# Kernel optimization log

Hardware: AMD Instinct MI355X
Metric: run time of the kernel (lower is better)

The kernel has to match this reference:

```python
import jax, jax.numpy as jnp
import numpy as np

CH = 64
INTER = 8  # max(64 // 8, 1)


def setup_inputs() -> dict:
    key = jax.random.key(0)
    ks = jax.random.split(key, 8)
    B, C, H, W = 4, CH, 64, 64
    x = jax.random.normal(ks[0], (B, C, H, W), dtype=jnp.float32)
    s = 1.0 / np.sqrt(C)
    Wq = jax.random.normal(ks[1], (INTER, C), dtype=jnp.float32) * s
    bq = jnp.zeros((INTER,), dtype=jnp.float32)
    Wk = jax.random.normal(ks[2], (INTER, C), dtype=jnp.float32) * s
    bk = jnp.zeros((INTER,), dtype=jnp.float32)
    Wv = jax.random.normal(ks[3], (C, C), dtype=jnp.float32) * s
    bv = jnp.zeros((C,), dtype=jnp.float32)
    gamma = jax.random.normal(ks[4], (1,), dtype=jnp.float32) * 0.1
    return {"x": x, "Wq": Wq, "bq": bq, "Wk": Wk, "bk": bk, "Wv": Wv, "bv": bv, "gamma": gamma}


def reference(x, Wq, bq, Wk, bk, Wv, bv, gamma):
    B, C, H, W = x.shape
    xf = x.reshape(B, C, H * W)  # [B, C, N]
    # 1x1 convs == per-pixel linear projections
    q = jnp.einsum('dc,bcn->bdn', Wq, xf) + bq[None, :, None]  # [B, d, N]
    k = jnp.einsum('dc,bcn->bdn', Wk, xf) + bk[None, :, None]  # [B, d, N]
    v = jnp.einsum('ec,bcn->ben', Wv, xf) + bv[None, :, None]  # [B, C, N]
    scale = 1.0 / np.sqrt(INTER).astype(np.float32)
    scores = jnp.einsum('bdi,bdj->bij', q, k) * scale  # [B, N, N]
    attn = jax.nn.softmax(scores, axis=-1)
    out = jnp.einsum('bcj,bij->bci', v, attn)  # value @ attn^T
    out = out.reshape(B, C, H, W)
    return gamma[0] * out + x
```

## Files before the change

### kernel.cpp

```cpp
#include <hip/hip_runtime.h>
#include <hip/hip_bf16.h>
#include <stdint.h>

#define BATCH 4
#define CCH   64
#define NPIX  4096
#define DQK   8

typedef __attribute__((ext_vector_type(8)))  short bf16x8;
typedef __attribute__((ext_vector_type(16))) float f32x16;

static __device__ __forceinline__ short f2bf(float f) {
    union { __hip_bfloat16 h; short s; } u;
    u.h = __float2bfloat16(f);
    return u.s;
}

__global__ __launch_bounds__(256) void proj_kernel(
    const float* __restrict__ x,
    const float* __restrict__ Wq, const float* __restrict__ bq,
    const float* __restrict__ Wk, const float* __restrict__ bk,
    const float* __restrict__ Wv, const float* __restrict__ bv,
    short* __restrict__ qo, short* __restrict__ ko, short* __restrict__ vo)
{
    __shared__ float xs[CCH][64];
    __shared__ float wv_s[CCH][CCH];
    __shared__ float wq_s[CCH][DQK];
    __shared__ float wk_s[CCH][DQK];

    const int b  = blockIdx.x >> 6;
    const int n0 = (blockIdx.x & 63) << 6;
    const int tid = threadIdx.x;

    for (int i = tid; i < CCH*CCH; i += 256) wv_s[i & 63][i >> 6] = Wv[i];
    for (int i = tid; i < CCH*DQK; i += 256) { wq_s[i & 63][i >> 6] = Wq[i]; wk_s[i & 63][i >> 6] = Wk[i]; }
    for (int i = tid; i < CCH*64; i += 256) {
        int c = i >> 6, p = i & 63;
        xs[c][p] = x[((size_t)b*CCH + c)*NPIX + n0 + p];
    }
    __syncthreads();

    const int p = tid & 63;
    const int g = tid >> 6;
    const int e0 = g * 16, d0 = g * 2;

    float av[16];
    #pragma unroll
    for (int i = 0; i < 16; ++i) av[i] = bv[e0 + i];
    float aq0 = bq[d0], aq1 = bq[d0+1];
    float ak0 = bk[d0], ak1 = bk[d0+1];

    for (int c = 0; c < CCH; ++c) {
        float xv = xs[c][p];
        const float4* wrow = (const float4*)&wv_s[c][e0];
        #pragma unroll
        for (int q4 = 0; q4 < 4; ++q4) {
            float4 w = wrow[q4];
            av[q4*4+0] += w.x * xv;
            av[q4*4+1] += w.y * xv;
            av[q4*4+2] += w.z * xv;
            av[q4*4+3] += w.w * xv;
        }
        float2 q2 = *(const float2*)&wq_s[c][d0];
        float2 k2 = *(const float2*)&wk_s[c][d0];
        aq0 += q2.x * xv; aq1 += q2.y * xv;
        ak0 += k2.x * xv; ak1 += k2.y * xv;
    }

    const float scale = 0.35355339059327373f;
    const size_t vb = (size_t)b * CCH * NPIX;
    #pragma unroll
    for (int i = 0; i < 16; ++i)
        vo[vb + (size_t)(e0 + i)*NPIX + n0 + p] = f2bf(av[i]);
    const size_t qb = ((size_t)b*NPIX + n0 + p)*DQK + d0;
    qo[qb]   = f2bf(aq0 * scale);
    qo[qb+1] = f2bf(aq1 * scale);
    ko[qb]   = f2bf(ak0);
    ko[qb+1] = f2bf(ak1);
}

__global__ __launch_bounds__(256) void attn_kernel(
    const short* __restrict__ qg, const short* __restrict__ kg,
    const short* __restrict__ vg,
    const float* __restrict__ x, const float* __restrict__ gamma,
    float* __restrict__ outp)
{
    __shared__ float m_s[4][32];
    __shared__ float l_s[4][32];
    __shared__ float acc_s[64][32];
    __shared__ __align__(16) short ps_s[4][32*40];

    const int b  = blockIdx.x >> 7;
    const int i0 = (blockIdx.x & 127) << 5;
    const int tid  = threadIdx.x;
    const int wave = tid >> 6, lane = tid & 63;
    const int hi = lane >> 5, li = lane & 31;

    for (int i = tid; i < 64*32; i += 256) acc_s[i >> 5][i & 31] = 0.f;
    __syncthreads();

    bf16x8 zf;
    #pragma unroll
    for (int i = 0; i < 8; ++i) zf[i] = 0;
    f32x16 z16;
    #pragma unroll
    for (int r = 0; r < 16; ++r) z16[r] = 0.f;

    bf16x8 qf = zf;
    if (hi == 0) qf = *(const bf16x8*)&qg[((size_t)b*NPIX + i0 + li)*DQK];

    f32x16 acc0 = z16, acc1 = z16;
    float m_run = -1e30f, l_run = 0.f;
    short* psb = &ps_s[wave][0];
    const size_t kbase = (size_t)b * NPIX * DQK;
    const size_t vbase = (size_t)b * CCH * NPIX;

    const int jbeg = wave << 10, jend = jbeg + 1024;
    for (int j0 = jbeg; j0 < jend; j0 += 32) {
        bf16x8 ak = zf;
        if (hi == 0) ak = *(const bf16x8*)&kg[kbase + (size_t)(j0 + li)*DQK];
        f32x16 S = __builtin_amdgcn_mfma_f32_32x32x16_bf16(ak, qf, z16, 0, 0, 0);

        float mx = S[0];
        #pragma unroll
        for (int r = 1; r < 16; ++r) mx = fmaxf(mx, S[r]);
        mx = fmaxf(mx, __shfl_xor(mx, 32));
        float m_new = fmaxf(m_run, mx);
        float fr = __expf(m_run - m_new);
        float p[16], ts = 0.f;
        #pragma unroll
        for (int r = 0; r < 16; ++r) { p[r] = __expf(S[r] - m_new); ts += p[r]; }
        ts += __shfl_xor(ts, 32);
        l_run = l_run * fr + ts;
        m_run = m_new;
        #pragma unroll
        for (int r = 0; r < 16; ++r) { acc0[r] *= fr; acc1[r] *= fr; }

        #pragma unroll
        for (int rp = 0; rp < 8; ++rp) {
            int r = rp * 2;
            int j = (r & 3) + ((r >> 2) << 3) + (hi << 2);
            uint32_t pk = (uint32_t)(uint16_t)f2bf(p[r]) |
                          ((uint32_t)(uint16_t)f2bf(p[r+1]) << 16);
            *(uint32_t*)((char*)psb + li*80 + j*2) = pk;
        }

        #pragma unroll
        for (int sub = 0; sub < 2; ++sub) {
            bf16x8 bp = *(const bf16x8*)((char*)psb + li*80 + (sub*16 + hi*8)*2);
            const short* vrow = &vg[vbase + (size_t)li*NPIX + j0 + sub*16 + hi*8];
            bf16x8 av0 = *(const bf16x8*)vrow;
            bf16x8 av1 = *(const bf16x8*)(vrow + (size_t)32*NPIX);
            acc0 = __builtin_amdgcn_mfma_f32_32x32x16_bf16(av0, bp, acc0, 0, 0, 0);
            acc1 = __builtin_amdgcn_mfma_f32_32x32x16_bf16(av1, bp, acc1, 0, 0, 0);
        }
    }

    if (hi == 0) { m_s[wave][li] = m_run; l_s[wave][li] = l_run; }
    __syncthreads();
    float M = fmaxf(fmaxf(m_s[0][li], m_s[1][li]), fmaxf(m_s[2][li], m_s[3][li]));
    float F = __expf(m_run - M);
    for (int w = 0; w < 4; ++w) {
        if (wave == w) {
            #pragma unroll
            for (int r = 0; r < 16; ++r) {
                int crow = (r & 3) + ((r >> 2) << 3) + (hi << 2);
                acc_s[crow][li]      += acc0[r] * F;
                acc_s[crow + 32][li] += acc1[r] * F;
            }
        }
        __syncthreads();
    }

    const float g0 = gamma[0];
    for (int idx = tid; idx < 64*32; idx += 256) {
        int c = idx >> 5, i = idx & 31;
        float Mq = fmaxf(fmaxf(m_s[0][i], m_s[1][i]), fmaxf(m_s[2][i], m_s[3][i]));
        float L = l_s[0][i]*__expf(m_s[0][i]-Mq) + l_s[1][i]*__expf(m_s[1][i]-Mq)
                + l_s[2][i]*__expf(m_s[2][i]-Mq) + l_s[3][i]*__expf(m_s[3][i]-Mq);
        size_t gidx = vbase + (size_t)c*NPIX + i0 + i;
        outp[gidx] = g0 * (acc_s[c][i] / L) + x[gidx];
    }
}

extern "C" void kernel_launch(void* const* d_in, const int* in_sizes, int n_in,
                              void* d_out, int out_size, void* d_ws, size_t ws_size,
                              hipStream_t stream) {
    const float* x     = (const float*)d_in[0];
    const float* Wq    = (const float*)d_in[1];
    const float* bq    = (const float*)d_in[2];
    const float* Wk    = (const float*)d_in[3];
    const float* bk    = (const float*)d_in[4];
    const float* Wv    = (const float*)d_in[5];
    const float* bv    = (const float*)d_in[6];
    const float* gamma = (const float*)d_in[7];

    short* qo = (short*)d_ws;
    short* ko = qo + (size_t)BATCH*NPIX*DQK;
    short* vo = ko + (size_t)BATCH*NPIX*DQK;

    proj_kernel<<<BATCH*(NPIX/64), 256, 0, stream>>>(x, Wq, bq, Wk, bk, Wv, bv, qo, ko, vo);
    attn_kernel<<<BATCH*(NPIX/32), 256, 0, stream>>>(qo, ko, vo, x, gamma, (float*)d_out);
}
```

Baseline: 126.3 us.

## Rewrite attention with lazy rescaling, exp2 folding, MFMA row sums and register P

Rewrites the attention kernel. The softmax scale times log2(e) is folded into q so exp2 can be used, and the running max is only updated when a score exceeds a threshold; the max offset is folded into the QK MFMA through an extra k column. P is packed to bf16 in registers and swapped across half-waves with permlane32_swap, which removes the LDS round trip. Row sums come from an extra MFMA against a ones vector. The block grows to 8 waves with a parallel cross-wave reduction in LDS, and the projection kernel is retiled to 32 pixels per block. The lazy-rescale threshold relies on scores staying bounded, which adds some numerical risk.

Measured after the change: 241.0 us. +90.8%, slower.

```diff
diff --git a/kernel.cpp b/kernel.cpp
--- a/kernel.cpp
+++ b/kernel.cpp
@@ -6,6 +6,7 @@
 #define CCH   64
 #define NPIX  4096
 #define DQK   8
+#define THR   8.0f
 
 typedef __attribute__((ext_vector_type(8)))  short bf16x8;
 typedef __attribute__((ext_vector_type(16))) float f32x16;
@@ -14,6 +15,16 @@
     union { __hip_bfloat16 h; short s; } u;
     u.h = __float2bfloat16(f);
     return u.s;
+}
+static __device__ __forceinline__ float bf2f(short s) {
+    union { unsigned u; float f; } x;
+    x.u = ((unsigned)(unsigned short)s) << 16;
+    return x.f;
+}
+static __device__ __forceinline__ uint32_t cvt_pk_bf16(float lo, float hi) {
+    uint32_t r;
+    asm("v_cvt_pk_bf16_f32 %0, %1, %2" : "=v"(r) : "v"(lo), "v"(hi));
+    return r;
 }
 
 __global__ __launch_bounds__(256) void proj_kernel(
@@ -23,72 +34,62 @@
     const float* __restrict__ Wv, const float* __restrict__ bv,
     short* __restrict__ qo, short* __restrict__ ko, short* __restrict__ vo)
 {
-    __shared__ float xs[CCH][64];
-    __shared__ float wv_s[CCH][CCH];
+    __shared__ float xs[CCH][32];
+    __shared__ float wv_s[CCH][68];
     __shared__ float wq_s[CCH][DQK];
     __shared__ float wk_s[CCH][DQK];
 
-    const int b  = blockIdx.x >> 6;
-    const int n0 = (blockIdx.x & 63) << 6;
+    const int b  = blockIdx.x >> 7;
+    const int n0 = (blockIdx.x & 127) << 5;
     const int tid = threadIdx.x;
 
     for (int i = tid; i < CCH*CCH; i += 256) wv_s[i & 63][i >> 6] = Wv[i];
     for (int i = tid; i < CCH*DQK; i += 256) { wq_s[i & 63][i >> 6] = Wq[i]; wk_s[i & 63][i >> 6] = Wk[i]; }
-    for (int i = tid; i < CCH*64; i += 256) {
-        int c = i >> 6, p = i & 63;
+    for (int i = tid; i < CCH*32; i += 256) {
+        int c = i >> 5, p = i & 31;
         xs[c][p] = x[((size_t)b*CCH + c)*NPIX + n0 + p];
     }
     __syncthreads();
 
-    const int p = tid & 63;
-    const int g = tid >> 6;
-    const int e0 = g * 16, d0 = g * 2;
-
-    float av[16];
-    #pragma unroll
-    for (int i = 0; i < 16; ++i) av[i] = bv[e0 + i];
-    float aq0 = bq[d0], aq1 = bq[d0+1];
-    float ak0 = bk[d0], ak1 = bk[d0+1];
+    const int p = tid & 31;
+    const int g = tid >> 5;
+    const int e0 = g * 8;
+
+    float av[8];
+    #pragma unroll
+    for (int i = 0; i < 8; ++i) av[i] = bv[e0 + i];
+    float aq = bq[g], akk = bk[g];
 
     for (int c = 0; c < CCH; ++c) {
         float xv = xs[c][p];
-        const float4* wrow = (const float4*)&wv_s[c][e0];
-        #pragma unroll
-        for (int q4 = 0; q4 < 4; ++q4) {
-            float4 w = wrow[q4];
-            av[q4*4+0] += w.x * xv;
-            av[q4*4+1] += w.y * xv;
-            av[q4*4+2] += w.z * xv;
-            av[q4*4+3] += w.w * xv;
-        }
-        float2 q2 = *(const float2*)&wq_s[c][d0];
-        float2 k2 = *(const float2*)&wk_s[c][d0];
-        aq0 += q2.x * xv; aq1 += q2.y * xv;
-        ak0 += k2.x * xv; ak1 += k2.y * xv;
-    }
-
-    const float scale = 0.35355339059327373f;
+        float4 w0 = *(const float4*)&wv_s[c][e0];
+        float4 w1 = *(const float4*)&wv_s[c][e0 + 4];
+        av[0] += w0.x*xv; av[1] += w0.y*xv; av[2] += w0.z*xv; av[3] += w0.w*xv;
+        av[4] += w1.x*xv; av[5] += w1.y*xv; av[6] += w1.z*xv; av[7] += w1.w*xv;
+        aq  += wq_s[c][g]*xv;
+        akk += wk_s[c][g]*xv;
+    }
+
+    const float qscale = 0.51010407112635f;
     const size_t vb = (size_t)b * CCH * NPIX;
     #pragma unroll
-    for (int i = 0; i < 16; ++i)
+    for (int i = 0; i < 8; ++i)
         vo[vb + (size_t)(e0 + i)*NPIX + n0 + p] = f2bf(av[i]);
-    const size_t qb = ((size_t)b*NPIX + n0 + p)*DQK + d0;
-    qo[qb]   = f2bf(aq0 * scale);
-    qo[qb+1] = f2bf(aq1 * scale);
-    ko[qb]   = f2bf(ak0);
-    ko[qb+1] = f2bf(ak1);
-}
-
-__global__ __launch_bounds__(256) void attn_kernel(
+    const size_t qb = ((size_t)b*NPIX + n0 + p)*DQK + g;
+    qo[qb] = f2bf(aq * qscale);
+    ko[qb] = f2bf(akk);
+}
+
+__global__ __launch_bounds__(512, 4) void attn_kernel(
     const short* __restrict__ qg, const short* __restrict__ kg,
     const short* __restrict__ vg,
     const float* __restrict__ x, const float* __restrict__ gamma,
     float* __restrict__ outp)
 {
-    __shared__ float m_s[4][32];
-    __shared__ float l_s[4][32];
-    __shared__ float acc_s[64][32];
-    __shared__ __align__(16) short ps_s[4][32*40];
+    __shared__ float m_s[8][32];
+    __shared__ float l_s[8][32];
+    __shared__ float linv_s[32];
+    __shared__ float acc_all[8][CCH][32];
 
     const int b  = blockIdx.x >> 7;
     const int i0 = (blockIdx.x & 127) << 5;
@@ -96,9 +97,6 @@
     const int wave = tid >> 6, lane = tid & 63;
     const int hi = lane >> 5, li = lane & 31;
 
-    for (int i = tid; i < 64*32; i += 256) acc_s[i >> 5][i & 31] = 0.f;
-    __syncthreads();
-
     bf16x8 zf;
     #pragma unroll
     for (int i = 0; i < 8; ++i) zf[i] = 0;
@@ -109,77 +107,111 @@
     bf16x8 qf = zf;
     if (hi == 0) qf = *(const bf16x8*)&qg[((size_t)b*NPIX + i0 + li)*DQK];
 
-    f32x16 acc0 = z16, acc1 = z16;
-    float m_run = -1e30f, l_run = 0.f;
-    short* psb = &ps_s[wave][0];
+    bf16x8 akf = zf;
+    if (hi == 1) akf[0] = (short)0x3F80;
+
+    bf16x8 ones;
+    #pragma unroll
+    for (int i = 0; i < 8; ++i) ones[i] = (short)0x3F80;
+
+    f32x16 acc0 = z16, acc1 = z16, accL = z16;
+    float m_run = 0.f;
+
     const size_t kbase = (size_t)b * NPIX * DQK;
     const size_t vbase = (size_t)b * CCH * NPIX;
-
-    const int jbeg = wave << 10, jend = jbeg + 1024;
-    for (int j0 = jbeg; j0 < jend; j0 += 32) {
-        bf16x8 ak = zf;
-        if (hi == 0) ak = *(const bf16x8*)&kg[kbase + (size_t)(j0 + li)*DQK];
-        f32x16 S = __builtin_amdgcn_mfma_f32_32x32x16_bf16(ak, qf, z16, 0, 0, 0);
-
-        float mx = S[0];
-        #pragma unroll
-        for (int r = 1; r < 16; ++r) mx = fmaxf(mx, S[r]);
-        mx = fmaxf(mx, __shfl_xor(mx, 32));
-        float m_new = fmaxf(m_run, mx);
-        float fr = __expf(m_run - m_new);
-        float p[16], ts = 0.f;
-        #pragma unroll
-        for (int r = 0; r < 16; ++r) { p[r] = __expf(S[r] - m_new); ts += p[r]; }
-        ts += __shfl_xor(ts, 32);
-        l_run = l_run * fr + ts;
-        m_run = m_new;
-        #pragma unroll
-        for (int r = 0; r < 16; ++r) { acc0[r] *= fr; acc1[r] *= fr; }
-
-        #pragma unroll
-        for (int rp = 0; rp < 8; ++rp) {
-            int r = rp * 2;
-            int j = (r & 3) + ((r >> 2) << 3) + (hi << 2);
-            uint32_t pk = (uint32_t)(uint16_t)f2bf(p[r]) |
-                          ((uint32_t)(uint16_t)f2bf(p[r+1]) << 16);
-            *(uint32_t*)((char*)psb + li*80 + j*2) = pk;
-        }
-
-        #pragma unroll
-        for (int sub = 0; sub < 2; ++sub) {
-            bf16x8 bp = *(const bf16x8*)((char*)psb + li*80 + (sub*16 + hi*8)*2);
-            const short* vrow = &vg[vbase + (size_t)li*NPIX + j0 + sub*16 + hi*8];
-            bf16x8 av0 = *(const bf16x8*)vrow;
-            bf16x8 av1 = *(const bf16x8*)(vrow + (size_t)32*NPIX);
-            acc0 = __builtin_amdgcn_mfma_f32_32x32x16_bf16(av0, bp, acc0, 0, 0, 0);
-            acc1 = __builtin_amdgcn_mfma_f32_32x32x16_bf16(av1, bp, acc1, 0, 0, 0);
-        }
-    }
-
-    if (hi == 0) { m_s[wave][li] = m_run; l_s[wave][li] = l_run; }
-    __syncthreads();
-    float M = fmaxf(fmaxf(m_s[0][li], m_s[1][li]), fmaxf(m_s[2][li], m_s[3][li]));
-    float F = __expf(m_run - M);
-    for (int w = 0; w < 4; ++w) {
-        if (wave == w) {
+    const short* vrow0 = &vg[vbase + (size_t)li*NPIX];
+    const short* vrow1 = vrow0 + (size_t)32*NPIX;
+
+    const int jbeg = wave << 9;
+    for (int t = 0; t < 16; ++t) {
+        const int j0 = jbeg + t*32;
+
+        if (hi == 0) akf = *(const bf16x8*)&kg[kbase + (size_t)(j0 + li)*DQK];
+        f32x16 S = __builtin_amdgcn_mfma_f32_32x32x16_bf16(akf, qf, z16, 0, 0, 0);
+
+        bf16x8 av00 = *(const bf16x8*)(vrow0 + j0 + hi*8);
+        bf16x8 av01 = *(const bf16x8*)(vrow0 + j0 + 16 + hi*8);
+        bf16x8 av10 = *(const bf16x8*)(vrow1 + j0 + hi*8);
+        bf16x8 av11 = *(const bf16x8*)(vrow1 + j0 + 16 + hi*8);
+
+        float mx = fmaxf(fmaxf(fmaxf(fmaxf(S[0],S[1]),fmaxf(S[2],S[3])),
+                               fmaxf(fmaxf(S[4],S[5]),fmaxf(S[6],S[7]))),
+                         fmaxf(fmaxf(fmaxf(S[8],S[9]),fmaxf(S[10],S[11])),
+                               fmaxf(fmaxf(S[12],S[13]),fmaxf(S[14],S[15]))));
+
+        if (__builtin_expect(__any(mx > THR), 0)) {
+            float mxp = fmaxf(mx, __shfl_xor(mx, 32));
+            float m_new  = m_run + fmaxf(mxp, 0.f);
+            float m_newr = bf2f(f2bf(m_new));
+            float dmr = m_newr - m_run;
+            float fr  = __builtin_amdgcn_exp2f(-dmr);
             #pragma unroll
             for (int r = 0; r < 16; ++r) {
-                int crow = (r & 3) + ((r >> 2) << 3) + (hi << 2);
-                acc_s[crow][li]      += acc0[r] * F;
-                acc_s[crow + 32][li] += acc1[r] * F;
+                S[r] = __builtin_amdgcn_exp2f(S[r] - dmr);
+                acc0[r] *= fr; acc1[r] *= fr;
             }
+            accL[0] *= fr;
+            m_run = m_newr;
+            if (hi == 1) qf[0] = f2bf(-m_newr);
+        } else {
+            #pragma unroll
+            for (int r = 0; r < 16; ++r) S[r] = __builtin_amdgcn_exp2f(S[r]);
         }
-        __syncthreads();
-    }
+
+        uint32_t a01 = cvt_pk_bf16(S[0], S[1]);
+        uint32_t a23 = cvt_pk_bf16(S[2], S[3]);
+        uint32_t a45 = cvt_pk_bf16(S[4], S[5]);
+        uint32_t a67 = cvt_pk_bf16(S[6], S[7]);
+        uint32_t a89 = cvt_pk_bf16(S[8], S[9]);
+        uint32_t aab = cvt_pk_bf16(S[10], S[11]);
+        uint32_t acd = cvt_pk_bf16(S[12], S[13]);
+        uint32_t aef = cvt_pk_bf16(S[14], S[15]);
+        asm("v_permlane32_swap_b32 %0, %1" : "+v"(a01), "+v"(a45));
+        asm("v_permlane32_swap_b32 %0, %1" : "+v"(a23), "+v"(a67));
+        asm("v_permlane32_swap_b32 %0, %1" : "+v"(a89), "+v"(acd));
+        asm("v_permlane32_swap_b32 %0, %1" : "+v"(aab), "+v"(aef));
+        union { uint32_t u[4]; bf16x8 v; } b0, b1;
+        b0.u[0] = a01; b0.u[1] = a23; b0.u[2] = a45; b0.u[3] = a67;
+        b1.u[0] = a89; b1.u[1] = aab; b1.u[2] = acd; b1.u[3] = aef;
+
+        acc0 = __builtin_amdgcn_mfma_f32_32x32x16_bf16(av00, b0.v, acc0, 0, 0, 0);
+        acc1 = __builtin_amdgcn_mfma_f32_32x32x16_bf16(av10, b0.v, acc1, 0, 0, 0);
+        accL = __builtin_amdgcn_mfma_f32_32x32x16_bf16(ones, b0.v, accL, 0, 0, 0);
+        acc0 = __builtin_amdgcn_mfma_f32_32x32x16_bf16(av01, b1.v, acc0, 0, 0, 0);
+        acc1 = __builtin_amdgcn_mfma_f32_32x32x16_bf16(av11, b1.v, acc1, 0, 0, 0);
+        accL = __builtin_amdgcn_mfma_f32_32x32x16_bf16(ones, b1.v, accL, 0, 0, 0);
+    }
+
+    if (hi == 0) { m_s[wave][li] = m_run; l_s[wave][li] = accL[0]; }
+    __syncthreads();
+
+    float M = m_s[0][li];
+    #pragma unroll
+    for (int w = 1; w < 8; ++w) M = fmaxf(M, m_s[w][li]);
+    float F = __builtin_amdgcn_exp2f(m_run - M);
+    #pragma unroll
+    for (int r = 0; r < 16; ++r) {
+        int row = (r & 3) + ((r >> 2) << 3) + (hi << 2);
+        acc_all[wave][row][li]      = acc0[r] * F;
+        acc_all[wave][row + 32][li] = acc1[r] * F;
+    }
+    if (wave == 0 && hi == 0) {
+        float L = 0.f;
+        #pragma unroll
+        for (int w = 0; w < 8; ++w)
+            L += l_s[w][li] * __builtin_amdgcn_exp2f(m_s[w][li] - M);
+        linv_s[li] = __builtin_amdgcn_rcpf(L);
+    }
+    __syncthreads();
 
     const float g0 = gamma[0];
-    for (int idx = tid; idx < 64*32; idx += 256) {
+    for (int idx = tid; idx < CCH*32; idx += 512) {
         int c = idx >> 5, i = idx & 31;
-        float Mq = fmaxf(fmaxf(m_s[0][i], m_s[1][i]), fmaxf(m_s[2][i], m_s[3][i]));
-        float L = l_s[0][i]*__expf(m_s[0][i]-Mq) + l_s[1][i]*__expf(m_s[1][i]-Mq)
-                + l_s[2][i]*__expf(m_s[2][i]-Mq) + l_s[3][i]*__expf(m_s[3][i]-Mq);
+        float s = 0.f;
+        #pragma unroll
+        for (int w = 0; w < 8; ++w) s += acc_all[w][c][i];
         size_t gidx = vbase + (size_t)c*NPIX + i0 + i;
-        outp[gidx] = g0 * (acc_s[c][i] / L) + x[gidx];
+        outp[gidx] = g0 * (s * linv_s[i]) + x[gidx];
     }
 }
 
@@ -199,6 +231,6 @@
     short* ko = qo + (size_t)BATCH*NPIX*DQK;
     short* vo = ko + (size_t)BATCH*NPIX*DQK;
 
-    proj_kernel<<<BATCH*(NPIX/64), 256, 0, stream>>>(x, Wq, bq, Wk, bk, Wv, bv, qo, ko, vo);
-    attn_kernel<<<BATCH*(NPIX/32), 256, 0, stream>>>(qo, ko, vo, x, gamma, (float*)d_out);
-}
+    proj_kernel<<<BATCH*(NPIX/32), 256, 0, stream>>>(x, Wq, bq, Wk, bk, Wv, bv, qo, ko, vo);
+    attn_kernel<<<BATCH*(NPIX/32), 512, 0, stream>>>(qo, ko, vo, x, gamma, (float*)d_out);
+}
```
